# Performance work log

Hardware: AMD Instinct MI355X
Metric: run time of the kernel (lower is better)

The kernel has to match this reference:

```python
import jax, jax.numpy as jnp
import numpy as np

# Dimensions: N sites, B batch, D bond dim, d physical dim, C output classes
N, B, D, d, C = 1024, 256, 16, 2, 10
STDDEV = 1e-5
INIT_DIAG = 1.0


def setup_inputs() -> dict:
    key = jax.random.key(0)
    k1, k2, k3 = jax.random.split(key, 3)
    x = jax.random.normal(k1, (N, B, d), dtype=jnp.float32)
    eye = jnp.eye(D, dtype=jnp.float32)
    # tensor[n,:,:,i] = init_diag * I + stddev * noise  (matches TF init)
    tensor = INIT_DIAG * eye[None, :, :, None] + STDDEV * jax.random.normal(k2, (N, D, D, d), dtype=jnp.float32)
    # Aout[c] = I + stddev * noise
    Aout = eye[None, :, :] + STDDEV * jax.random.normal(k3, (C, D, D), dtype=jnp.float32)
    return {"x": x, "tensor": tensor, "Aout": Aout}


def _chain_prod(A):
    # A: (n, b, D, D) -> ordered matrix-chain product (b, D, D), log-depth tree.
    # Faithful to parallel_contract: pairwise einsum per level; odd leftover is
    # kept at the end of the list (order-preserving, associativity-equivalent).
    while A.shape[0] > 1:
        n = A.shape[0]
        half = n // 2
        prod = jnp.einsum('nblk,nbkr->nblr', A[0:2 * half:2], A[1:2 * half:2])
        if n % 2 == 1:
            prod = jnp.concatenate([prod, A[-1:]], axis=0)
        A = prod
    return A[0]


def reference(x, tensor, Aout):
    # A: (N, B, D, D) site matrices after contracting input features
    A = jnp.einsum('nbi,nlri->nblr', x, tensor)
    nhalf = A.shape[0] // 2
    # Left half product, take row 0 (left boundary); right half, take col 0
    Al = _chain_prod(A[:nhalf])[:, 0, :]   # (B, D)
    Ar = _chain_prod(A[nhalf:])[:, :, 0]   # (B, D)
    # out[b,o] = Al[b] @ Aout[o] @ Ar[b]
    return jnp.einsum('bl,olr,br->bo', Al, Aout, Ar)
```

## Files before the change

### kernel.cpp

```cpp
#include <hip/hip_runtime.h>


#define BATCH  256
#define NCLS   10
#define NSITES 1024
#define NGRP   16
#define SEGLEN 8
#define NB     8

typedef __attribute__((ext_vector_type(4))) float f32x4;
typedef __attribute__((ext_vector_type(2))) float f32x2;
typedef __attribute__((ext_vector_type(4))) short short4b;
typedef __attribute__((ext_vector_type(2))) unsigned uint2v;
typedef __attribute__((ext_vector_type(4))) unsigned short us4;
typedef __attribute__((ext_vector_type(8))) short short8;

static __device__ __forceinline__ unsigned short bf16tr(float f) {
    return (unsigned short)(__builtin_bit_cast(unsigned, f) >> 16);
}
static __device__ __forceinline__ float bf16tof(unsigned short h) {
    return __builtin_bit_cast(float, (unsigned)h << 16);
}
static __device__ __forceinline__ unsigned fbits(float f) {
    return __builtin_bit_cast(unsigned, f);
}
static __device__ __forceinline__ unsigned pkhi(float hi, float lo) {
    return __builtin_amdgcn_perm(fbits(hi), fbits(lo), 0x07060302u);
}
static __device__ __forceinline__ short4b mk4(unsigned lo, unsigned hi) {
    uint2v u; u.x = lo; u.y = hi;
    return __builtin_bit_cast(short4b, u);
}
static __device__ __forceinline__ f32x4 mfma16(short4b a, short4b b, f32x4 c) {
#if __has_builtin(__builtin_amdgcn_mfma_f32_16x16x16bf16_1k)
    return __builtin_amdgcn_mfma_f32_16x16x16bf16_1k(a, b, c, 0, 0, 0);
#else
    f32x4 d;
    asm volatile("v_mfma_f32_16x16x16_bf16 %0, %1, %2, %3"
                 : "=v"(d) : "v"(a), "v"(b), "v"(c));
    return d;
#endif
}

__global__ __launch_bounds__(512, 4) void chain_kernel(
    const float* __restrict__ x,
    const float* __restrict__ tensor,
    unsigned short* __restrict__ M2)
{
    __shared__ __align__(16) unsigned short stg[64 * 256];
    const int t = threadIdx.x, w = t >> 6, lane = t & 63;
    const int quad = lane >> 4, l15 = lane & 15;
    const int bt = blockIdx.x & 31, o = blockIdx.x >> 5;
    const int b0 = bt * NB;
    const int seg = o * 8 + w, n0 = seg * SEGLEN;

    f32x4 d[NB];
#pragma unroll
    for (int j = 0; j < NB; ++j)
#pragma unroll
        for (int r = 0; r < 4; ++r) d[j][r] = (quad * 4 + r == l15) ? 1.0f : 0.0f;

    const float* __restrict__ tb =
        tensor + (size_t)n0 * 512 + ((size_t)(4 * quad) * 16 + l15) * 2;

    f32x2 v0 = __builtin_bit_cast(f32x2, *(const float2*)(tb));
    f32x2 v1 = __builtin_bit_cast(f32x2, *(const float2*)(tb + 32));
    f32x2 v2 = __builtin_bit_cast(f32x2, *(const float2*)(tb + 64));
    f32x2 v3 = __builtin_bit_cast(f32x2, *(const float2*)(tb + 96));
    float4 xq0, xq1, xq2, xq3;
    {
        const float4* __restrict__ xp = (const float4*)(x + (size_t)n0 * BATCH * 2 + b0 * 2);
        xq0 = xp[0]; xq1 = xp[1]; xq2 = xp[2]; xq3 = xp[3];
    }

#pragma unroll
    for (int s = 0; s < SEGLEN; ++s) {
        f32x2 nv0, nv1, nv2, nv3;
        float4 nxq0, nxq1, nxq2, nxq3;
        if (s + 1 < SEGLEN) {
            const float* __restrict__ tsn = tb + (size_t)(s + 1) * 512;
            nv0 = __builtin_bit_cast(f32x2, *(const float2*)(tsn));
            nv1 = __builtin_bit_cast(f32x2, *(const float2*)(tsn + 32));
            nv2 = __builtin_bit_cast(f32x2, *(const float2*)(tsn + 64));
            nv3 = __builtin_bit_cast(f32x2, *(const float2*)(tsn + 96));
            const float4* __restrict__ xpn =
                (const float4*)(x + ((size_t)(n0 + s + 1) * BATCH + b0) * 2);
            nxq0 = xpn[0]; nxq1 = xpn[1]; nxq2 = xpn[2]; nxq3 = xpn[3];
        }
        const float xs0[NB] = {xq0.x, xq0.z, xq1.x, xq1.z, xq2.x, xq2.z, xq3.x, xq3.z};
        const float xs1[NB] = {xq0.y, xq0.w, xq1.y, xq1.w, xq2.y, xq2.w, xq3.y, xq3.w};
#pragma unroll
        for (int j = 0; j < NB; ++j) {
            const f32x2 xv = {xs0[j], xs1[j]};
            const f32x2 p0 = v0 * xv;
            const f32x2 p1 = v1 * xv;
            const f32x2 p2 = v2 * xv;
            const f32x2 p3 = v3 * xv;
            const float a0 = p0[0] + p0[1];
            const float a1 = p1[0] + p1[1];
            const float a2 = p2[0] + p2[1];
            const float a3 = p3[0] + p3[1];
            const short4b af = mk4(pkhi(a1, a0), pkhi(a3, a2));
            const short4b wb = mk4(pkhi(d[j][1], d[j][0]), pkhi(d[j][3], d[j][2]));
            f32x4 c0 = {0.0f, 0.0f, 0.0f, 0.0f};
            d[j] = mfma16(af, wb, c0);
        }
        if (s + 1 < SEGLEN) {
            v0 = nv0; v1 = nv1; v2 = nv2; v3 = nv3;
            xq0 = nxq0; xq1 = nxq1; xq2 = nxq2; xq3 = nxq3;
        }
    }

    if (w & 1) {
#pragma unroll
        for (int j = 0; j < NB; ++j) {
            const int sl = j * 8 + w;
#pragma unroll
            for (int r = 0; r < 4; ++r)
                stg[sl * 256 + (quad * 4 + r) * 16 + l15] = bf16tr(d[j][r]);
        }
    } else {
#pragma unroll
        for (int j = 0; j < NB; ++j) {
            const int sl = j * 8 + w;
            us4 pk = {bf16tr(d[j][0]), bf16tr(d[j][1]), bf16tr(d[j][2]), bf16tr(d[j][3])};
            *(us4*)(stg + sl * 256 + l15 * 16 + quad * 4) = pk;
        }
    }
    __syncthreads();

    short4b af1v[4], bf1v[4];
#pragma unroll
    for (int i = 0; i < 4; ++i) {
        const int p = 4 * w + i, j = p >> 2, h = p & 3;
        af1v[i] = __builtin_bit_cast(short4b,
            *(const uint2v*)(stg + (j * 8 + 2 * h + 1) * 256 + l15 * 16 + quad * 4));
        bf1v[i] = __builtin_bit_cast(short4b,
            *(const uint2v*)(stg + (j * 8 + 2 * h) * 256 + l15 * 16 + quad * 4));
    }
    __syncthreads();
#pragma unroll
    for (int i = 0; i < 4; ++i) {
        const int p = 4 * w + i, j = p >> 2, h = p & 3;
        f32x4 c0 = {0.0f, 0.0f, 0.0f, 0.0f};
        f32x4 q = mfma16(af1v[i], bf1v[i], c0);
        const int sl = j * 8 + h;
        if (h & 1) {
#pragma unroll
            for (int r = 0; r < 4; ++r)
                stg[sl * 256 + (quad * 4 + r) * 16 + l15] = bf16tr(q[r]);
        } else {
            us4 pk = {bf16tr(q[0]), bf16tr(q[1]), bf16tr(q[2]), bf16tr(q[3])};
            *(us4*)(stg + sl * 256 + l15 * 16 + quad * 4) = pk;
        }
    }
    __syncthreads();

    short4b af2v[2], bf2v[2];
#pragma unroll
    for (int i = 0; i < 2; ++i) {
        const int p = 2 * w + i, j = p >> 1, k = p & 1;
        af2v[i] = __builtin_bit_cast(short4b,
            *(const uint2v*)(stg + (j * 8 + 2 * k + 1) * 256 + l15 * 16 + quad * 4));
        bf2v[i] = __builtin_bit_cast(short4b,
            *(const uint2v*)(stg + (j * 8 + 2 * k) * 256 + l15 * 16 + quad * 4));
    }
    __syncthreads();
#pragma unroll
    for (int i = 0; i < 2; ++i) {
        const int p = 2 * w + i, j = p >> 1, k = p & 1;
        f32x4 c0 = {0.0f, 0.0f, 0.0f, 0.0f};
        f32x4 r = mfma16(af2v[i], bf2v[i], c0);
        const int sl = j * 8 + k;
        if (k) {
#pragma unroll
            for (int rr = 0; rr < 4; ++rr)
                stg[sl * 256 + (quad * 4 + rr) * 16 + l15] = bf16tr(r[rr]);
        } else {
            us4 pk = {bf16tr(r[0]), bf16tr(r[1]), bf16tr(r[2]), bf16tr(r[3])};
            *(us4*)(stg + sl * 256 + l15 * 16 + quad * 4) = pk;
        }
    }
    __syncthreads();

    {
        const int j = w;
        const short4b af3 = __builtin_bit_cast(short4b,
            *(const uint2v*)(stg + (j * 8 + 1) * 256 + l15 * 16 + quad * 4));
        const short4b bf3 = __builtin_bit_cast(short4b,
            *(const uint2v*)(stg + (j * 8 + 0) * 256 + l15 * 16 + quad * 4));
        f32x4 c0 = {0.0f, 0.0f, 0.0f, 0.0f};
        f32x4 rr = mfma16(af3, bf3, c0);
        us4 pk = {bf16tr(rr[0]), bf16tr(rr[1]), bf16tr(rr[2]), bf16tr(rr[3])};
        *(us4*)(M2 + ((size_t)(b0 + j) * NGRP + o) * 256 + l15 * 16 + quad * 4) = pk;
    }
}

__global__ __launch_bounds__(256) void combine_kernel(
    const unsigned short* __restrict__ M2,
    const float* __restrict__ Aout,
    float* __restrict__ out)
{
    __shared__ __align__(16) unsigned short rm[16 * 256];
    __shared__ __align__(16) unsigned short cm[16 * 256];
    const int b = blockIdx.x, t = threadIdx.x;
    const int wave = t >> 6, lane = t & 63, quad = lane >> 4, l15 = lane & 15;

    const short8* __restrict__ src = (const short8*)(M2 + (size_t)b * NGRP * 256);
#pragma unroll
    for (int i2 = 0; i2 < 2; ++i2) {
        const int i = t + 256 * i2;
        const short8 v = src[i];
        *((short8*)cm + i) = v;
        const int mat = i >> 5, c = (i >> 1) & 15, r0 = (i & 1) * 8;
#pragma unroll
        for (int e = 0; e < 8; ++e)
            rm[mat * 256 + (r0 + e) * 16 + c] = (unsigned short)v[e];
    }
    __syncthreads();

    for (int lvl = 0; lvl < 3; ++lvl) {
        const int np = 8 >> lvl;
        short4b afr[2], bfr[2];
        int pids[2], nmine = 0;
        for (int p = wave; p < np; p += 4) {
            afr[nmine] = __builtin_bit_cast(short4b,
                 *(const uint2v*)(rm + (2 * p + 1) * 256 + l15 * 16 + quad * 4));
            bfr[nmine] = __builtin_bit_cast(short4b,
                 *(const uint2v*)(cm + (2 * p) * 256 + l15 * 16 + quad * 4));
            pids[nmine] = p; ++nmine;
        }
        __syncthreads();
        for (int ii = 0; ii < nmine; ++ii) {
            f32x4 c0 = {0.0f, 0.0f, 0.0f, 0.0f};
            f32x4 r = mfma16(afr[ii], bfr[ii], c0);
            const int p = pids[ii];
#pragma unroll
            for (int rr = 0; rr < 4; ++rr)
                rm[p * 256 + (quad * 4 + rr) * 16 + l15] = bf16tr(r[rr]);
            us4 pk = {bf16tr(r[0]), bf16tr(r[1]), bf16tr(r[2]), bf16tr(r[3])};
            *(us4*)(cm + p * 256 + l15 * 16 + quad * 4) = pk;
        }
        __syncthreads();
    }

    if (t < NCLS * 16) {
        const int o = t >> 4, r = t & 15;
        const float vr = bf16tof(rm[256 + r]);
        float s = 0.0f;
#pragma unroll
        for (int l = 0; l < 16; ++l)
            s = __builtin_fmaf(bf16tof(rm[l * 16]), Aout[((size_t)o * 16 + l) * 16 + r], s);
        s *= vr;
#pragma unroll
        for (int off = 8; off > 0; off >>= 1)
            s += __shfl_xor(s, off, 16);
        if (r == 0) out[(size_t)b * NCLS + o] = s;
    }
}

extern "C" void kernel_launch(void* const* d_in, const int* in_sizes, int n_in,
                              void* d_out, int out_size, void* d_ws, size_t ws_size,
                              hipStream_t stream)
{
    const float* x      = (const float*)d_in[0];
    const float* tensor = (const float*)d_in[1];
    const float* Aout   = (const float*)d_in[2];
    float* out = (float*)d_out;

    unsigned short* M2 = (unsigned short*)d_ws;

    chain_kernel<<<(NSITES / (SEGLEN * 8)) * (BATCH / NB), 512, 0, stream>>>(x, tensor, M2);
    combine_kernel<<<BATCH, 256, 0, stream>>>(M2, Aout, out);
}
```

Baseline: 73.61 us.

## Restructure reduction trees to keep products in registers with fewer block barriers

The post-segment pairwise reduction in the chain kernel now has each wave reduce its own batch element's eight segment products. It feeds MFMA results back as the B operand directly from registers (packD) and uses small per-wave LDS scratch for the A operand, replacing three block-wide barrier rounds. The combine kernel similarly uses one shared buffer with a wave-local two-level reduction and fewer __syncthreads. This cuts barrier and LDS round-trip overhead, at the cost of extra LDS (the Q buffer) that may reduce occupancy, and less parallelism per reduction level.

```diff
diff --git a/kernel.cpp b/kernel.cpp
--- a/kernel.cpp
+++ b/kernel.cpp
@@ -30,6 +30,9 @@
 static __device__ __forceinline__ short4b mk4(unsigned lo, unsigned hi) {
     uint2v u; u.x = lo; u.y = hi;
     return __builtin_bit_cast(short4b, u);
+}
+static __device__ __forceinline__ short4b packD(f32x4 d) {
+    return mk4(pkhi(d[1], d[0]), pkhi(d[3], d[2]));
 }
 static __device__ __forceinline__ f32x4 mfma16(short4b a, short4b b, f32x4 c) {
 #if __has_builtin(__builtin_amdgcn_mfma_f32_16x16x16bf16_1k)
@@ -47,8 +50,10 @@
     const float* __restrict__ tensor,
     unsigned short* __restrict__ M2)
 {
-    __shared__ __align__(16) unsigned short stg[64 * 256];
-    const int t = threadIdx.x, w = t >> 6, lane = t & 63;
+    __shared__ __align__(16) unsigned short S[64 * 256];
+    __shared__ __align__(16) unsigned short Q[24 * 256];
+    const int t = threadIdx.x, lane = t & 63;
+    const int w = __builtin_amdgcn_readfirstlane(t >> 6);
     const int quad = lane >> 4, l15 = lane & 15;
     const int bt = blockIdx.x & 31, o = blockIdx.x >> 5;
     const int b0 = bt * NB;
@@ -69,7 +74,7 @@
     f32x2 v3 = __builtin_bit_cast(f32x2, *(const float2*)(tb + 96));
     float4 xq0, xq1, xq2, xq3;
     {
-        const float4* __restrict__ xp = (const float4*)(x + (size_t)n0 * BATCH * 2 + b0 * 2);
+        const float4* __restrict__ xp = (const float4*)(x + ((size_t)n0 * BATCH + b0) * 2);
         xq0 = xp[0]; xq1 = xp[1]; xq2 = xp[2]; xq3 = xp[3];
     }
 
@@ -101,9 +106,8 @@
             const float a2 = p2[0] + p2[1];
             const float a3 = p3[0] + p3[1];
             const short4b af = mk4(pkhi(a1, a0), pkhi(a3, a2));
-            const short4b wb = mk4(pkhi(d[j][1], d[j][0]), pkhi(d[j][3], d[j][2]));
             f32x4 c0 = {0.0f, 0.0f, 0.0f, 0.0f};
-            d[j] = mfma16(af, wb, c0);
+            d[j] = mfma16(af, packD(d[j]), c0);
         }
         if (s + 1 < SEGLEN) {
             v0 = nv0; v1 = nv1; v2 = nv2; v3 = nv3;
@@ -117,82 +121,51 @@
             const int sl = j * 8 + w;
 #pragma unroll
             for (int r = 0; r < 4; ++r)
-                stg[sl * 256 + (quad * 4 + r) * 16 + l15] = bf16tr(d[j][r]);
+                S[sl * 256 + (quad * 4 + r) * 16 + l15] = bf16tr(d[j][r]);
         }
     } else {
 #pragma unroll
         for (int j = 0; j < NB; ++j) {
             const int sl = j * 8 + w;
             us4 pk = {bf16tr(d[j][0]), bf16tr(d[j][1]), bf16tr(d[j][2]), bf16tr(d[j][3])};
-            *(us4*)(stg + sl * 256 + l15 * 16 + quad * 4) = pk;
-        }
-    }
-    __syncthreads();
-
-    short4b af1v[4], bf1v[4];
-#pragma unroll
-    for (int i = 0; i < 4; ++i) {
-        const int p = 4 * w + i, j = p >> 2, h = p & 3;
-        af1v[i] = __builtin_bit_cast(short4b,
-            *(const uint2v*)(stg + (j * 8 + 2 * h + 1) * 256 + l15 * 16 + quad * 4));
-        bf1v[i] = __builtin_bit_cast(short4b,
-            *(const uint2v*)(stg + (j * 8 + 2 * h) * 256 + l15 * 16 + quad * 4));
-    }
-    __syncthreads();
-#pragma unroll
-    for (int i = 0; i < 4; ++i) {
-        const int p = 4 * w + i, j = p >> 2, h = p & 3;
-        f32x4 c0 = {0.0f, 0.0f, 0.0f, 0.0f};
-        f32x4 q = mfma16(af1v[i], bf1v[i], c0);
-        const int sl = j * 8 + h;
-        if (h & 1) {
-#pragma unroll
-            for (int r = 0; r < 4; ++r)
-                stg[sl * 256 + (quad * 4 + r) * 16 + l15] = bf16tr(q[r]);
-        } else {
-            us4 pk = {bf16tr(q[0]), bf16tr(q[1]), bf16tr(q[2]), bf16tr(q[3])};
-            *(us4*)(stg + sl * 256 + l15 * 16 + quad * 4) = pk;
-        }
-    }
-    __syncthreads();
-
-    short4b af2v[2], bf2v[2];
-#pragma unroll
-    for (int i = 0; i < 2; ++i) {
-        const int p = 2 * w + i, j = p >> 1, k = p & 1;
-        af2v[i] = __builtin_bit_cast(short4b,
-            *(const uint2v*)(stg + (j * 8 + 2 * k + 1) * 256 + l15 * 16 + quad * 4));
-        bf2v[i] = __builtin_bit_cast(short4b,
-            *(const uint2v*)(stg + (j * 8 + 2 * k) * 256 + l15 * 16 + quad * 4));
-    }
-    __syncthreads();
-#pragma unroll
-    for (int i = 0; i < 2; ++i) {
-        const int p = 2 * w + i, j = p >> 1, k = p & 1;
-        f32x4 c0 = {0.0f, 0.0f, 0.0f, 0.0f};
-        f32x4 r = mfma16(af2v[i], bf2v[i], c0);
-        const int sl = j * 8 + k;
-        if (k) {
-#pragma unroll
-            for (int rr = 0; rr < 4; ++rr)
-                stg[sl * 256 + (quad * 4 + rr) * 16 + l15] = bf16tr(r[rr]);
-        } else {
-            us4 pk = {bf16tr(r[0]), bf16tr(r[1]), bf16tr(r[2]), bf16tr(r[3])};
-            *(us4*)(stg + sl * 256 + l15 * 16 + quad * 4) = pk;
+            *(us4*)(S + sl * 256 + l15 * 16 + quad * 4) = pk;
         }
     }
     __syncthreads();
 
     {
-        const int j = w;
+        const f32x4 z = {0.0f, 0.0f, 0.0f, 0.0f};
+        f32x4 q[4];
+#pragma unroll
+        for (int h = 0; h < 4; ++h) {
+            const short4b af = __builtin_bit_cast(short4b,
+                *(const uint2v*)(S + (w * 8 + 2 * h + 1) * 256 + l15 * 16 + quad * 4));
+            const short4b bf = __builtin_bit_cast(short4b,
+                *(const uint2v*)(S + (w * 8 + 2 * h) * 256 + l15 * 16 + quad * 4));
+            q[h] = mfma16(af, bf, z);
+        }
+        unsigned short* const sc0 = Q + w * 256;
+        unsigned short* const sc1 = Q + (8 + w) * 256;
+#pragma unroll
+        for (int r = 0; r < 4; ++r) {
+            sc0[(quad * 4 + r) * 16 + l15] = bf16tr(q[1][r]);
+            sc1[(quad * 4 + r) * 16 + l15] = bf16tr(q[3][r]);
+        }
+        const short4b afr0 = __builtin_bit_cast(short4b,
+            *(const uint2v*)(sc0 + l15 * 16 + quad * 4));
+        const short4b afr1 = __builtin_bit_cast(short4b,
+            *(const uint2v*)(sc1 + l15 * 16 + quad * 4));
+        const f32x4 r0 = mfma16(afr0, packD(q[0]), z);
+        const f32x4 r1 = mfma16(afr1, packD(q[2]), z);
+        unsigned short* const sc2 = Q + (16 + w) * 256;
+#pragma unroll
+        for (int r = 0; r < 4; ++r)
+            sc2[(quad * 4 + r) * 16 + l15] = bf16tr(r1[r]);
         const short4b af3 = __builtin_bit_cast(short4b,
-            *(const uint2v*)(stg + (j * 8 + 1) * 256 + l15 * 16 + quad * 4));
-        const short4b bf3 = __builtin_bit_cast(short4b,
-            *(const uint2v*)(stg + (j * 8 + 0) * 256 + l15 * 16 + quad * 4));
-        f32x4 c0 = {0.0f, 0.0f, 0.0f, 0.0f};
-        f32x4 rr = mfma16(af3, bf3, c0);
+            *(const uint2v*)(sc2 + l15 * 16 + quad * 4));
+        const f32x4 rr = mfma16(af3, packD(r0), z);
         us4 pk = {bf16tr(rr[0]), bf16tr(rr[1]), bf16tr(rr[2]), bf16tr(rr[3])};
-        *(us4*)(M2 + ((size_t)(b0 + j) * NGRP + o) * 256 + l15 * 16 + quad * 4) = pk;
+        *(us4*)(M2 + ((size_t)(b0 + w) * NGRP + o) * 256 + l15 * 16 + quad * 4) = pk;
     }
 }
 
@@ -201,56 +174,78 @@
     const float* __restrict__ Aout,
     float* __restrict__ out)
 {
-    __shared__ __align__(16) unsigned short rm[16 * 256];
-    __shared__ __align__(16) unsigned short cm[16 * 256];
-    const int b = blockIdx.x, t = threadIdx.x;
-    const int wave = t >> 6, lane = t & 63, quad = lane >> 4, l15 = lane & 15;
+    __shared__ __align__(16) unsigned short S[16 * 256];
+    const int b = blockIdx.x, t = threadIdx.x, lane = t & 63;
+    const int w = __builtin_amdgcn_readfirstlane(t >> 6);
+    const int quad = lane >> 4, l15 = lane & 15;
 
     const short8* __restrict__ src = (const short8*)(M2 + (size_t)b * NGRP * 256);
 #pragma unroll
     for (int i2 = 0; i2 < 2; ++i2) {
         const int i = t + 256 * i2;
         const short8 v = src[i];
-        *((short8*)cm + i) = v;
-        const int mat = i >> 5, c = (i >> 1) & 15, r0 = (i & 1) * 8;
-#pragma unroll
-        for (int e = 0; e < 8; ++e)
-            rm[mat * 256 + (r0 + e) * 16 + c] = (unsigned short)v[e];
-    }
-    __syncthreads();
-
-    for (int lvl = 0; lvl < 3; ++lvl) {
-        const int np = 8 >> lvl;
-        short4b afr[2], bfr[2];
-        int pids[2], nmine = 0;
-        for (int p = wave; p < np; p += 4) {
-            afr[nmine] = __builtin_bit_cast(short4b,
-                 *(const uint2v*)(rm + (2 * p + 1) * 256 + l15 * 16 + quad * 4));
-            bfr[nmine] = __builtin_bit_cast(short4b,
-                 *(const uint2v*)(cm + (2 * p) * 256 + l15 * 16 + quad * 4));
-            pids[nmine] = p; ++nmine;
-        }
-        __syncthreads();
-        for (int ii = 0; ii < nmine; ++ii) {
-            f32x4 c0 = {0.0f, 0.0f, 0.0f, 0.0f};
-            f32x4 r = mfma16(afr[ii], bfr[ii], c0);
-            const int p = pids[ii];
-#pragma unroll
-            for (int rr = 0; rr < 4; ++rr)
-                rm[p * 256 + (quad * 4 + rr) * 16 + l15] = bf16tr(r[rr]);
-            us4 pk = {bf16tr(r[0]), bf16tr(r[1]), bf16tr(r[2]), bf16tr(r[3])};
-            *(us4*)(cm + p * 256 + l15 * 16 + quad * 4) = pk;
-        }
-        __syncthreads();
-    }
+        const int mat = i >> 5;
+        if (mat & 1) {
+            const int c = (i >> 1) & 15, r0 = (i & 1) * 8;
+#pragma unroll
+            for (int e = 0; e < 8; ++e)
+                S[mat * 256 + (r0 + e) * 16 + c] = (unsigned short)v[e];
+        } else {
+            *((short8*)S + i) = v;
+        }
+    }
+    __syncthreads();
+
+    const f32x4 z = {0.0f, 0.0f, 0.0f, 0.0f};
+    {
+        const short4b afA = __builtin_bit_cast(short4b,
+            *(const uint2v*)(S + (4 * w + 1) * 256 + l15 * 16 + quad * 4));
+        const short4b bfA = __builtin_bit_cast(short4b,
+            *(const uint2v*)(S + (4 * w + 0) * 256 + l15 * 16 + quad * 4));
+        const short4b afB = __builtin_bit_cast(short4b,
+            *(const uint2v*)(S + (4 * w + 3) * 256 + l15 * 16 + quad * 4));
+        const short4b bfB = __builtin_bit_cast(short4b,
+            *(const uint2v*)(S + (4 * w + 2) * 256 + l15 * 16 + quad * 4));
+        const f32x4 q0 = mfma16(afA, bfA, z);
+        const f32x4 q1 = mfma16(afB, bfB, z);
+        unsigned short* const sc = S + (4 * w + 1) * 256;
+#pragma unroll
+        for (int r = 0; r < 4; ++r)
+            sc[(quad * 4 + r) * 16 + l15] = bf16tr(q1[r]);
+        const short4b af2 = __builtin_bit_cast(short4b,
+            *(const uint2v*)(sc + l15 * 16 + quad * 4));
+        const f32x4 l2 = mfma16(af2, packD(q0), z);
+        if (w & 1) {
+#pragma unroll
+            for (int r = 0; r < 4; ++r)
+                S[(4 * w) * 256 + (quad * 4 + r) * 16 + l15] = bf16tr(l2[r]);
+        } else {
+            us4 pk = {bf16tr(l2[0]), bf16tr(l2[1]), bf16tr(l2[2]), bf16tr(l2[3])};
+            *(us4*)(S + (4 * w) * 256 + l15 * 16 + quad * 4) = pk;
+        }
+    }
+    __syncthreads();
+
+    if (w < 2) {
+        const short4b af = __builtin_bit_cast(short4b,
+            *(const uint2v*)(S + (4 * (2 * w + 1)) * 256 + l15 * 16 + quad * 4));
+        const short4b bf = __builtin_bit_cast(short4b,
+            *(const uint2v*)(S + (4 * (2 * w)) * 256 + l15 * 16 + quad * 4));
+        const f32x4 f = mfma16(af, bf, z);
+#pragma unroll
+        for (int r = 0; r < 4; ++r)
+            S[(2 + w) * 256 + (quad * 4 + r) * 16 + l15] = bf16tr(f[r]);
+    }
+    __syncthreads();
 
     if (t < NCLS * 16) {
         const int o = t >> 4, r = t & 15;
-        const float vr = bf16tof(rm[256 + r]);
+        const float vr = bf16tof(S[3 * 256 + r]);
         float s = 0.0f;
 #pragma unroll
         for (int l = 0; l < 16; ++l)
-            s = __builtin_fmaf(bf16tof(rm[l * 16]), Aout[((size_t)o * 16 + l) * 16 + r], s);
+            s = __builtin_fmaf(bf16tof(S[2 * 256 + l * 16]),
+                               Aout[((size_t)o * 16 + l) * 16 + r], s);
         s *= vr;
 #pragma unroll
         for (int off = 8; off > 0; off >>= 1)
```

Result: no change. 73.10 us (-0.7%).
